# Optimization experiments

Hardware: AMD Instinct MI355X
Metric: run time of the kernel (lower is better)

The kernel has to match this reference:

```python
import jax, jax.numpy as jnp
import numpy as np

N = 65536          # particles
E = 524288         # relations (avg degree 8)
RIG = 4096         # rigid instance = particles [0, RIG); fluid = [RIG, N)
PSTEPS = 2
ATTR, STATE, RELD, NF = 3, 6, 1, 128
DT = 1.0 / 60.0
MEAN_P = np.zeros(3, np.float32); STD_P = np.ones(3, np.float32)
MEAN_V = np.zeros(3, np.float32); STD_V = np.ones(3, np.float32)


def _lin(x, w, b):
    return x @ w.T + b  # torch Linear convention: w is [out, in]


def setup_inputs() -> dict:
    key = jax.random.key(0)
    ks = iter(jax.random.split(key, 40))
    d = {}
    d["state"] = jax.random.normal(next(ks), (N, STATE), jnp.float32)
    d["attr"] = jax.random.normal(next(ks), (N, ATTR), jnp.float32)
    d["Ra"] = jax.random.normal(next(ks), (E, RELD), jnp.float32)
    d["rel_recv"] = jax.random.randint(next(ks), (E,), 0, N, jnp.int32)
    d["rel_send"] = jax.random.randint(next(ks), (E,), 0, N, jnp.int32)

    def w(shape):
        return jax.random.normal(next(ks), shape, jnp.float32) / np.sqrt(shape[1])

    d["pe_w0"] = w((NF, ATTR + 2 * STATE)); d["pe_b0"] = jnp.zeros(NF)
    d["pe_w1"] = w((NF, NF)); d["pe_b1"] = jnp.zeros(NF)
    d["re_w0"] = w((NF, 2 * ATTR + 4 * STATE + RELD)); d["re_b0"] = jnp.zeros(NF)
    d["re_w1"] = w((NF, NF)); d["re_b1"] = jnp.zeros(NF)
    d["re_w2"] = w((NF, NF)); d["re_b2"] = jnp.zeros(NF)
    d["rp_w"] = w((NF, 3 * NF)); d["rp_b"] = jnp.zeros(NF)
    d["pp_w"] = w((NF, 2 * NF)); d["pp_b"] = jnp.zeros(NF)
    d["rg_w0"] = w((NF, NF)); d["rg_b0"] = jnp.zeros(NF)
    d["rg_w1"] = w((NF, NF)); d["rg_b1"] = jnp.zeros(NF)
    d["rg_w2"] = w((7, NF)); d["rg_b2"] = jnp.zeros(7)
    d["fl_w0"] = w((NF, NF)); d["fl_b0"] = jnp.zeros(NF)
    d["fl_w1"] = w((NF, NF)); d["fl_b1"] = jnp.zeros(NF)
    d["fl_w2"] = w((3, NF)); d["fl_b2"] = jnp.zeros(3)
    return d


def reference(state, attr, Ra, rel_recv, rel_send,
              pe_w0, pe_b0, pe_w1, pe_b1,
              re_w0, re_b0, re_w1, re_b1, re_w2, re_b2,
              rp_w, rp_b, pp_w, pp_b,
              rg_w0, rg_b0, rg_w1, rg_b1, rg_w2, rg_b2,
              fl_w0, fl_b0, fl_w1, fl_b1, fl_w2, fl_b2):
    relu = jax.nn.relu
    mean_p = jnp.asarray(MEAN_P); std_p = jnp.asarray(STD_P)
    mean_v = jnp.asarray(MEAN_V); std_v = jnp.asarray(STD_V)

    # rigid-body offset (state minus instance centroid for the rigid instance)
    offset = jnp.zeros_like(state).at[:RIG].set(
        state[:RIG] - jnp.mean(state[:RIG], axis=0))
    attr2 = jnp.concatenate([attr, offset], axis=1)        # [N, ATTR+STATE]

    # f_O^enc: particle encoder on [attr2, state]
    pe_in = jnp.concatenate([attr2, state], axis=1)         # [N, 15]
    particle_encode = relu(_lin(relu(_lin(pe_in, pe_w0, pe_b0)), pe_w1, pe_b1))

    # f_R^enc: relation encoder on gathered receiver/sender features
    rel_in = jnp.concatenate([attr2[rel_recv], attr2[rel_send],
                              state[rel_recv], state[rel_send], Ra], axis=1)  # [E, 31]
    h = relu(_lin(rel_in, re_w0, re_b0))
    h = relu(_lin(h, re_w1, re_b1))
    relation_encode = relu(_lin(h, re_w2, re_b2))           # [E, NF]

    # propagation: gather effects -> f_R -> scatter-add -> f_O
    effect = jnp.zeros((N, NF), state.dtype)
    for _ in range(PSTEPS):
        r_eff = effect[rel_recv]                            # [E, NF]
        s_eff = effect[rel_send]                            # [E, NF]
        rel_eff = relu(_lin(jnp.concatenate(
            [relation_encode, r_eff, s_eff], axis=1), rp_w, rp_b))
        agg = jax.ops.segment_sum(rel_eff, rel_recv, num_segments=N)  # Rr @ rel_eff
        effect = relu(_lin(jnp.concatenate(
            [particle_encode, agg], axis=1), pp_w, pp_b))   # residual=False

    # rigid predictor: quaternion + translation of the rigid body
    pooled = jnp.mean(effect[:RIG], axis=0)                 # [NF]
    t = _lin(relu(_lin(relu(_lin(pooled, rg_w0, rg_b0)), rg_w1, rg_b1)), rg_w2, rg_b2)
    q = t[:4] / jnp.linalg.norm(t[:4])
    w, x, y, z = q[0], q[1], q[2], q[3]
    R = jnp.stack([
        jnp.stack([1.0 - 2 * (y * y + z * z), 2 * (x * y + z * w), 2 * (x * z - y * w)]),
        jnp.stack([2 * (x * y - z * w), 1.0 - 2 * (x * x + z * z), 2 * (y * z + x * w)]),
        jnp.stack([2 * (x * z + y * w), 2 * (y * z - x * w), 1.0 - 2 * (x * x + y * y)]),
    ])
    b = t[4:] * std_p
    p0 = state[:RIG, :3] * std_p + mean_p
    c = jnp.mean(p0, axis=0)
    p1 = (p0 - c) @ R + b + c
    v = (p1 - p0) / DT
    pred_rigid = (v - mean_v) / std_v                       # [RIG, 3]

    # fluid predictor: per-particle MLP
    f = relu(_lin(effect[RIG:], fl_w0, fl_b0))
    f = relu(_lin(f, fl_w1, fl_b1))
    pred_fluid = _lin(f, fl_w2, fl_b2)                      # [N-RIG, 3]

    return jnp.concatenate([pred_rigid, pred_fluid], axis=0)  # [N, 3]
```

## Files before the change

### kernel.cpp

```cpp
#include <hip/hip_runtime.h>
#include <hip/hip_bf16.h>
#include <cstdio>

#define N_P   65536
#define N_E   524288
#define RIG_  4096

typedef __attribute__((ext_vector_type(8))) short bf16x8;
typedef __attribute__((ext_vector_type(4))) float f32x4;
typedef unsigned short u16;
typedef unsigned int   u32;

__device__ __forceinline__ u16 f2b(float x) {
    __hip_bfloat16 h = __float2bfloat16(x);
    return *(u16*)&h;
}
__device__ __forceinline__ float b2f(u16 u) {
    union { unsigned u; float f; } c; c.u = ((unsigned)u) << 16; return c.f;
}
__device__ __forceinline__ unsigned pk2(float x, float y) {
    return (unsigned)f2b(x) | ((unsigned)f2b(y) << 16);
}
#define MFMA(a,b,c) __builtin_amdgcn_mfma_f32_16x16x32_bf16((a),(b),(c),0,0,0)

__device__ __forceinline__ void bar_l() {
    asm volatile("s_waitcnt lgkmcnt(0)\n\ts_barrier" ::: "memory");
}

__global__ __launch_bounds__(256) void k_hist(const int* __restrict__ recv,
                                              u32* __restrict__ cnt) {
    int i = blockIdx.x * 256 + threadIdx.x;
    if (i < N_E) atomicAdd(&cnt[recv[i]], 1u);
}
__global__ __launch_bounds__(256) void k_scan1(u32* __restrict__ data,
                                               u32* __restrict__ bsum) {
    __shared__ u32 s[256];
    int t = threadIdx.x, g = blockIdx.x * 256 + t;
    u32 v = data[g];
    s[t] = v; __syncthreads();
    for (int o = 1; o < 256; o <<= 1) {
        u32 x = (t >= o) ? s[t - o] : 0u;
        __syncthreads(); s[t] += x; __syncthreads();
    }
    data[g] = s[t] - v;
    if (t == 255) bsum[blockIdx.x] = s[255];
}
__global__ __launch_bounds__(256) void k_scan2(u32* __restrict__ bsum) {
    __shared__ u32 s[256];
    int t = threadIdx.x;
    u32 v = bsum[t];
    s[t] = v; __syncthreads();
    for (int o = 1; o < 256; o <<= 1) {
        u32 x = (t >= o) ? s[t - o] : 0u;
        __syncthreads(); s[t] += x; __syncthreads();
    }
    bsum[t] = s[t] - v;
}
__global__ __launch_bounds__(256) void k_scan3(u32* __restrict__ data,
                                               const u32* __restrict__ bsum) {
    int g = blockIdx.x * 256 + threadIdx.x;
    data[g] += bsum[blockIdx.x];
}
__global__ __launch_bounds__(256) void k_scatter(const int* __restrict__ recv,
                                                 const int* __restrict__ send,
                                                 u32* __restrict__ head,
                                                 int4* __restrict__ edges) {
    int i = blockIdx.x * 256 + threadIdx.x;
    if (i < N_E) {
        int n = recv[i];
        u32 pos = atomicAdd(&head[n], 1u);
        edges[pos] = make_int4(n, send[i], i, 0);
    }
}

struct CvtJob { const float* src; u16* dst; int n; int mode; int bstart; };
struct CvtArgs { CvtJob j[14]; };

__global__ __launch_bounds__(256) void k_cvt_all(CvtArgs a) {
    int b = blockIdx.x;
    int ji = 0;
    #pragma unroll
    for (int k = 1; k < 14; k++) if (b >= a.j[k].bstart) ji = k;
    CvtJob jb = a.j[ji];
    int i = (b - jb.bstart) * 256 + threadIdx.x;
    if (i >= jb.n) return;
    if (jb.mode == 0) {
        jb.dst[i] = f2b(jb.src[i]);
    } else if (jb.mode == 2) {
        int r = i >> 7;
        jb.dst[i] = (r < 3) ? f2b(jb.src[i]) : 0;
    } else if (jb.mode == 3) {
        int r = i >> 7, c = i & 127;
        jb.dst[i] = f2b(jb.src[r * 384 + c]);
    } else if (jb.mode == 4) {
        int r = i >> 7, c = i & 127;
        jb.dst[i] = f2b(jb.src[r * 256 + c]);
    } else if (jb.mode == 5) {
        int r = i >> 5, c = i & 31;
        float v = 0.f;
        if (c < 9)       v = jb.src[r * 31 + c];
        else if (c < 15) v = jb.src[r * 31 + 18 + (c - 9)];
        jb.dst[i] = f2b(v);
    } else if (jb.mode == 6) {
        int r = i >> 5, c = i & 31;
        float v = 0.f;
        if (c < 9)       v = jb.src[r * 31 + 9 + c];
        else if (c < 15) v = jb.src[r * 31 + 24 + (c - 9)];
        jb.dst[i] = f2b(v);
    } else {
        int r = i >> 5, c = i & 31;
        jb.dst[i] = (c < 15) ? f2b(jb.src[r * 15 + c]) : 0;
    }
}

__global__ __launch_bounds__(256) void k_centroid(const float* __restrict__ state,
                                                  float* __restrict__ cent) {
    int d = blockIdx.x;
    __shared__ float red[256];
    float s = 0.f;
    for (int r = threadIdx.x; r < RIG_; r += 256) s += state[r * 6 + d];
    red[threadIdx.x] = s; __syncthreads();
    for (int o = 128; o > 0; o >>= 1) {
        if (threadIdx.x < o) red[threadIdx.x] += red[threadIdx.x + o];
        __syncthreads();
    }
    if (threadIdx.x == 0) cent[d] = red[0] / (float)RIG_;
}

__global__ __launch_bounds__(512, 4) void k_particle_ext(
        const float* __restrict__ state, const float* __restrict__ attr,
        const float* __restrict__ cent,
        const u16* __restrict__ w0r, const u16* __restrict__ w0s,
        const u16* __restrict__ pew0, const float* __restrict__ pe_b0,
        const u16* __restrict__ pew1, const float* __restrict__ pe_b1,
        const u16* __restrict__ wp,
        u16* __restrict__ P, u16* __restrict__ Q, u16* __restrict__ T) {
    __shared__ float in_s[64][16];
    __shared__ u16 INF[64 * 32];
    __shared__ __align__(16) u16 BUFA[64 * 128];
    __shared__ __align__(16) u16 BUFB[64 * 128];
    int t = threadIdx.x;
    int w = t >> 6, lane = t & 63, mm = lane & 15, quad = lane >> 4;
    int colw = w * 16 + mm;
    bf16x8 W0Rf = *(const bf16x8*)(w0r  + (size_t)colw * 32 + quad * 8);
    bf16x8 W0Sf = *(const bf16x8*)(w0s  + (size_t)colw * 32 + quad * 8);
    bf16x8 PE0f = *(const bf16x8*)(pew0 + (size_t)colw * 32 + quad * 8);
    bf16x8 PE1f[4], WPf[4];
    #pragma unroll
    for (int kc = 0; kc < 4; kc++) {
        PE1f[kc] = *(const bf16x8*)(pew1 + (size_t)colw * 128 + kc * 32 + quad * 8);
        WPf[kc]  = *(const bf16x8*)(wp   + (size_t)colw * 128 + kc * 32 + quad * 8);
    }
    float b0c = pe_b0[colw], b1c = pe_b1[colw];
    const int NTL = N_P / 64;
    for (int tile = blockIdx.x; tile < NTL; tile += gridDim.x) {
        int base = tile * 64;
        bar_l();
        for (int it = t; it < 64 * 15; it += 512) {
            int r = it / 15, c = it % 15;
            int p = base + r;
            float v;
            if (c < 3)      v = attr[p * 3 + c];
            else if (c < 9) v = (p < RIG_) ? (state[p * 6 + (c - 3)] - cent[c - 3]) : 0.0f;
            else            v = state[p * 6 + (c - 9)];
            in_s[r][c] = v;
        }
        bar_l();
        if (t < 256) {
            int wv = t >> 6, kq4 = (t >> 4) & 3, m = t & 15;
            int e = wv * 16 + m;
            u16 tmp[8];
            #pragma unroll
            for (int j = 0; j < 8; j++) {
                int k = kq4 * 8 + j;
                tmp[j] = (k < 15) ? f2b(in_s[e][k]) : (u16)0;
            }
            *(uint4*)&INF[((wv * 4 + kq4) * 16 + m) * 8] = *(uint4*)tmp;
        }
        bar_l();
        bf16x8 af0[4];
        #pragma unroll
        for (int eg = 0; eg < 4; eg++)
            af0[eg] = *(const bf16x8*)&INF[((eg * 4 + quad) * 16 + mm) * 8];
        {
            f32x4 a[4] = {};
            #pragma unroll
            for (int eg = 0; eg < 4; eg++) a[eg] = MFMA(af0[eg], W0Rf, a[eg]);
            #pragma unroll
            for (int eg = 0; eg < 4; eg++)
                #pragma unroll
                for (int rg = 0; rg < 4; rg++)
                    P[(size_t)(base + eg * 16 + quad * 4 + rg) * 128 + colw] = f2b(a[eg][rg]);
        }
        {
            f32x4 a[4] = {};
            #pragma unroll
            for (int eg = 0; eg < 4; eg++) a[eg] = MFMA(af0[eg], W0Sf, a[eg]);
            #pragma unroll
            for (int eg = 0; eg < 4; eg++)
                #pragma unroll
                for (int rg = 0; rg < 4; rg++)
                    Q[(size_t)(base + eg * 16 + quad * 4 + rg) * 128 + colw] = f2b(a[eg][rg]);
        }
        {
            f32x4 a[4] = {};
            #pragma unroll
            for (int eg = 0; eg < 4; eg++) a[eg] = MFMA(af0[eg], PE0f, a[eg]);
            #pragma unroll
            for (int eg = 0; eg < 4; eg++)
                #pragma unroll
                for (int rg = 0; rg < 4; rg++)
                    BUFA[((eg * 16 + (colw >> 3)) * 16 + quad * 4 + rg) * 8 + (colw & 7)] =
                        f2b(fmaxf(a[eg][rg] + b0c, 0.f));
        }
        bar_l();
        {
            f32x4 a[4] = {};
            #pragma unroll
            for (int eg = 0; eg < 4; eg++)
                #pragma unroll
                for (int kc = 0; kc < 4; kc++) {
                    bf16x8 af = *(const bf16x8*)&BUFA[((eg * 16 + kc * 4 + quad) * 16 + mm) * 8];
                    a[eg] = MFMA(af, PE1f[kc], a[eg]);
                }
            #pragma unroll
            for (int eg = 0; eg < 4; eg++)
                #pragma unroll
                for (int rg = 0; rg < 4; rg++)
                    BUFB[((eg * 16 + (colw >> 3)) * 16 + quad * 4 + rg) * 8 + (colw & 7)] =
                        f2b(fmaxf(a[eg][rg] + b1c, 0.f));
        }
        bar_l();
        {
            f32x4 a[4] = {};
            #pragma unroll
            for (int eg = 0; eg < 4; eg++)
                #pragma unroll
                for (int kc = 0; kc < 4; kc++) {
                    bf16x8 af = *(const bf16x8*)&BUFB[((eg * 16 + kc * 4 + quad) * 16 + mm) * 8];
                    a[eg] = MFMA(af, WPf[kc], a[eg]);
                }
            #pragma unroll
            for (int eg = 0; eg < 4; eg++)
                #pragma unroll
                for (int rg = 0; rg < 4; rg++)
                    T[(size_t)(base + eg * 16 + quad * 4 + rg) * 128 + colw] = f2b(a[eg][rg]);
        }
    }
}

__global__ __launch_bounds__(512, 4) void k_rel(
        const u16* __restrict__ P, const u16* __restrict__ Q,
        const float* __restrict__ Ra, const int4* __restrict__ edges,
        const float* __restrict__ re_w0_raw, const float* __restrict__ b0,
        const u16* __restrict__ w1b, const float* __restrict__ b1,
        const u16* __restrict__ w2b, const float* __restrict__ b2,
        const u16* __restrict__ wreb, const float* __restrict__ rpb,
        u16* __restrict__ Z, float* __restrict__ agg) {
    __shared__ __align__(16) u16 BUFA[64 * 136];
    __shared__ __align__(16) u16 BUFB[64 * 136];
    __shared__ int rv_s[2][64];
    __shared__ float wRa_s[128], b0_s[128], rpb_s[128];
    int t = threadIdx.x;
    if (t < 128) {
        wRa_s[t] = re_w0_raw[t * 31 + 30];
        b0_s[t] = b0[t]; rpb_s[t] = rpb[t];
    }
    int w = t >> 6, lane = t & 63, mm = lane & 15, quad = lane >> 4;
    int colw = w * 16 + mm;
    bf16x8 W1f[4], W2f[4], WEf[4];
    #pragma unroll
    for (int kc = 0; kc < 4; kc++) {
        W1f[kc] = *(const bf16x8*)(w1b  + (size_t)colw * 128 + kc * 32 + quad * 8);
        W2f[kc] = *(const bf16x8*)(w2b  + (size_t)colw * 128 + kc * 32 + quad * 8);
        WEf[kc] = *(const bf16x8*)(wreb + (size_t)colw * 128 + kc * 32 + quad * 8);
    }
    float b1c = b1[colw], b2c = b2[colw];
    int es = t >> 3, cs2 = (t & 7) * 2;
    int egs = es >> 4, ms = es & 15;
    int sseg = t >> 7, cseg = t & 127;
    int zrow = t >> 3, zc0 = (t & 7) * 16;
    const long NT = N_E / 64;
    const long stride = gridDim.x;

    long tile = blockIdx.x;
    uint4 upC0, upC1, uqC0, uqC1; float raC; int rvC;
    {
        long nb = tile * 64;
        int4 e = edges[nb + es];
        rvC = edges[nb + (t & 63)].x;
        raC = Ra[e.z];
        upC0 = *(const uint4*)(P + (size_t)e.x * 128 + (size_t)cs2 * 8);
        upC1 = *(const uint4*)(P + (size_t)e.x * 128 + (size_t)(cs2 + 1) * 8);
        uqC0 = *(const uint4*)(Q + (size_t)e.y * 128 + (size_t)cs2 * 8);
        uqC1 = *(const uint4*)(Q + (size_t)e.y * 128 + (size_t)(cs2 + 1) * 8);
    }
    __syncthreads();
    int p = 0;
    for (; tile < NT; tile += stride) {
        long base = tile * 64;
        long ntile = tile + stride;
        bool hn = ntile < NT;
        int4 eN = make_int4(0, 0, 0, 0); int rvN = 0;
        if (hn) {
            long nb = ntile * 64;
            eN  = edges[nb + es];
            rvN = edges[nb + (t & 63)].x;
        }
        if (t < 64) rv_s[p][t] = rvC;
        {
            #pragma unroll
            for (int ci = 0; ci < 2; ci++) {
                int kq = cs2 + ci;
                uint4 up = ci ? upC1 : upC0;
                uint4 uq = ci ? uqC1 : uqC0;
                const u16* pp = (const u16*)&up; const u16* qq = (const u16*)&uq;
                u16 outv[8];
                #pragma unroll
                for (int j = 0; j < 8; j++) {
                    int c = kq * 8 + j;
                    float v = b2f(pp[j]) + b2f(qq[j]) + raC * wRa_s[c] + b0_s[c];
                    outv[j] = f2b(fmaxf(v, 0.f));
                }
                *(uint4*)&BUFA[((egs * 16 + kq) * 16 + ms) * 8] = *(uint4*)outv;
            }
        }
        bar_l();
        uint4 upN0{}, upN1{}, uqN0{}, uqN1{}; float raN = 0.f;
        if (hn) {
            raN  = Ra[eN.z];
            upN0 = *(const uint4*)(P + (size_t)eN.x * 128 + (size_t)cs2 * 8);
            upN1 = *(const uint4*)(P + (size_t)eN.x * 128 + (size_t)(cs2 + 1) * 8);
            uqN0 = *(const uint4*)(Q + (size_t)eN.y * 128 + (size_t)cs2 * 8);
            uqN1 = *(const uint4*)(Q + (size_t)eN.y * 128 + (size_t)(cs2 + 1) * 8);
        }
        {
            f32x4 acc[4] = {};
            #pragma unroll
            for (int eg = 0; eg < 4; eg++)
                #pragma unroll
                for (int kc = 0; kc < 4; kc++) {
                    bf16x8 af = *(const bf16x8*)&BUFA[((eg * 16 + kc * 4 + quad) * 16 + mm) * 8];
                    acc[eg] = MFMA(af, W1f[kc], acc[eg]);
                }
            #pragma unroll
            for (int eg = 0; eg < 4; eg++)
                #pragma unroll
                for (int rg = 0; rg < 4; rg++)
                    BUFB[((eg * 16 + (colw >> 3)) * 16 + quad * 4 + rg) * 8 + (colw & 7)] =
                        f2b(fmaxf(acc[eg][rg] + b1c, 0.f));
        }
        bar_l();
        {
            f32x4 acc[4] = {};
            #pragma unroll
            for (int eg = 0; eg < 4; eg++)
                #pragma unroll
                for (int kc = 0; kc < 4; kc++) {
                    bf16x8 af = *(const bf16x8*)&BUFB[((eg * 16 + kc * 4 + quad) * 16 + mm) * 8];
                    acc[eg] = MFMA(af, W2f[kc], acc[eg]);
                }
            #pragma unroll
            for (int eg = 0; eg < 4; eg++)
                #pragma unroll
                for (int rg = 0; rg < 4; rg++)
                    BUFA[((eg * 16 + (colw >> 3)) * 16 + quad * 4 + rg) * 8 + (colw & 7)] =
                        f2b(fmaxf(acc[eg][rg] + b2c, 0.f));
        }
        bar_l();
        {
            f32x4 zacc[4] = {};
            #pragma unroll
            for (int eg = 0; eg < 4; eg++)
                #pragma unroll
                for (int kc = 0; kc < 4; kc++) {
                    bf16x8 af = *(const bf16x8*)&BUFA[((eg * 16 + kc * 4 + quad) * 16 + mm) * 8];
                    zacc[eg] = MFMA(af, WEf[kc], zacc[eg]);
                }
            #pragma unroll
            for (int eg = 0; eg < 4; eg++)
                #pragma unroll
                for (int rg = 0; rg < 4; rg++)
                    BUFB[(eg * 16 + quad * 4 + rg) * 136 + colw] = f2b(zacc[eg][rg]);
        }
        bar_l();
        {
            uint4 z0 = *(const uint4*)&BUFB[zrow * 136 + zc0];
            uint4 z1 = *(const uint4*)&BUFB[zrow * 136 + zc0 + 8];
            *(uint4*)&Z[(base + zrow) * 128 + zc0]     = z0;
            *(uint4*)&Z[(base + zrow) * 128 + zc0 + 8] = z1;
        }
        {
            int r0 = sseg * 16;
            int cur = rv_s[p][r0];
            float a = fmaxf(b2f(BUFB[r0 * 136 + cseg]) + rpb_s[cseg], 0.f);
            bool first = true;
            for (int rr = r0 + 1; rr < r0 + 16; rr++) {
                int n = rv_s[p][rr];
                float v = fmaxf(b2f(BUFB[rr * 136 + cseg]) + rpb_s[cseg], 0.f);
                if (n == cur) a += v;
                else {
                    if (first) atomicAdd(&agg[(size_t)cur * 128 + cseg], a);
                    else       agg[(size_t)cur * 128 + cseg] = a;
                    first = false; cur = n; a = v;
                }
            }
            atomicAdd(&agg[(size_t)cur * 128 + cseg], a);
        }
        if (hn) { upC0 = upN0; upC1 = upN1; uqC0 = uqN0; uqC1 = uqN1; raC = raN; rvC = rvN; }
        p ^= 1;
    }
}

__global__ __launch_bounds__(512, 4) void k_node2(
        const float* __restrict__ agg, const u16* __restrict__ T,
        const u16* __restrict__ wab, const float* __restrict__ ppb,
        const u16* __restrict__ wrb, const u16* __restrict__ wsb,
        u16* __restrict__ U, u16* __restrict__ V) {
    __shared__ __align__(16) u16 BUFA[64 * 128];
    __shared__ __align__(16) u16 BUFB[64 * 128];
    int t = threadIdx.x;
    int w = t >> 6, lane = t & 63, mm = lane & 15, quad = lane >> 4;
    int colw = w * 16 + mm;
    bf16x8 WAf[4], WRf[4], WSf[4];
    #pragma unroll
    for (int kc = 0; kc < 4; kc++) {
        WAf[kc] = *(const bf16x8*)(wab + (size_t)colw * 128 + kc * 32 + quad * 8);
        WRf[kc] = *(const bf16x8*)(wrb + (size_t)colw * 128 + kc * 32 + quad * 8);
        WSf[kc] = *(const bf16x8*)(wsb + (size_t)colw * 128 + kc * 32 + quad * 8);
    }
    float ppbc = ppb[colw];
    int es = t >> 3, cs2 = (t & 7) * 2;
    int egs = es >> 4, ms = es & 15;
    const int NTL = N_P / 64;
    for (int tile = blockIdx.x; tile < NTL; tile += gridDim.x) {
        long base = (long)tile * 64;
        __syncthreads();
        #pragma unroll
        for (int ci = 0; ci < 2; ci++) {
            int kq = cs2 + ci;
            const float* src = agg + (base + es) * 128 + kq * 8;
            float4 f0 = *(const float4*)src, f1 = *(const float4*)(src + 4);
            uint4 v;
            v.x = pk2(f0.x, f0.y); v.y = pk2(f0.z, f0.w);
            v.z = pk2(f1.x, f1.y); v.w = pk2(f1.z, f1.w);
            *(uint4*)&BUFA[((egs * 16 + kq) * 16 + ms) * 8] = v;
        }
        bar_l();
        {
            f32x4 acc[4] = {};
            #pragma unroll
            for (int eg = 0; eg < 4; eg++)
                #pragma unroll
                for (int kc = 0; kc < 4; kc++) {
                    bf16x8 af = *(const bf16x8*)&BUFA[((eg * 16 + kc * 4 + quad) * 16 + mm) * 8];
                    acc[eg] = MFMA(af, WAf[kc], acc[eg]);
                }
            #pragma unroll
            for (int eg = 0; eg < 4; eg++)
                #pragma unroll
                for (int rg = 0; rg < 4; rg++) {
                    long row = base + eg * 16 + quad * 4 + rg;
                    float v = acc[eg][rg] + b2f(T[row * 128 + colw]) + ppbc;
                    BUFB[((eg * 16 + (colw >> 3)) * 16 + quad * 4 + rg) * 8 + (colw & 7)] =
                        f2b(fmaxf(v, 0.f));
                }
        }
        bar_l();
        {
            f32x4 au[4] = {}, av[4] = {};
            #pragma unroll
            for (int eg = 0; eg < 4; eg++)
                #pragma unroll
                for (int kc = 0; kc < 4; kc++) {
                    bf16x8 af = *(const bf16x8*)&BUFB[((eg * 16 + kc * 4 + quad) * 16 + mm) * 8];
                    au[eg] = MFMA(af, WRf[kc], au[eg]);
                    av[eg] = MFMA(af, WSf[kc], av[eg]);
                }
            #pragma unroll
            for (int eg = 0; eg < 4; eg++)
                #pragma unroll
                for (int rg = 0; rg < 4; rg++) {
                    long row = base + eg * 16 + quad * 4 + rg;
                    U[row * 128 + colw] = f2b(au[eg][rg]);
                    V[row * 128 + colw] = f2b(av[eg][rg]);
                }
        }
    }
}

__global__ __launch_bounds__(512, 4) void k_node2fl(
        const float* __restrict__ agg, const u16* __restrict__ T,
        const u16* __restrict__ wab, const float* __restrict__ ppb,
        float* __restrict__ pooledsum,
        const u16* __restrict__ w0b, const float* __restrict__ b0,
        const u16* __restrict__ w1b, const float* __restrict__ b1,
        const u16* __restrict__ w2b, const float* __restrict__ b2,
        float* __restrict__ out) {
    __shared__ __align__(16) u16 BUFA[64 * 128];
    __shared__ __align__(16) u16 BUFB[64 * 128];
    int t = threadIdx.x;
    int w = t >> 6, lane = t & 63, mm = lane & 15, quad = lane >> 4;
    int colw = w * 16 + mm;
    bf16x8 WAf[4], W0f[4], W1f[4];
    #pragma unroll
    for (int kc = 0; kc < 4; kc++) {
        WAf[kc] = *(const bf16x8*)(wab + (size_t)colw * 128 + kc * 32 + quad * 8);
        W0f[kc] = *(const bf16x8*)(w0b + (size_t)colw * 128 + kc * 32 + quad * 8);
        W1f[kc] = *(const bf16x8*)(w1b + (size_t)colw * 128 + kc * 32 + quad * 8);
    }
    float ppbc = ppb[colw], b0c = b0[colw], b1c = b1[colw];
    int es = t >> 3, cs2 = (t & 7) * 2;
    int egs = es >> 4, ms = es & 15;
    const int NTL = N_P / 64;
    for (int tile = blockIdx.x; tile < NTL; tile += gridDim.x) {
        long base = (long)tile * 64;
        bool fluid = base >= RIG_;
        bar_l();
        #pragma unroll
        for (int ci = 0; ci < 2; ci++) {
            int kq = cs2 + ci;
            const float* src = agg + (base + es) * 128 + kq * 8;
            float4 f0 = *(const float4*)src, f1 = *(const float4*)(src + 4);
            uint4 v;
            v.x = pk2(f0.x, f0.y); v.y = pk2(f0.z, f0.w);
            v.z = pk2(f1.x, f1.y); v.w = pk2(f1.z, f1.w);
            *(uint4*)&BUFA[((egs * 16 + kq) * 16 + ms) * 8] = v;
        }
        bar_l();
        f32x4 acc[4] = {};
        #pragma unroll
        for (int eg = 0; eg < 4; eg++)
            #pragma unroll
            for (int kc = 0; kc < 4; kc++) {
                bf16x8 af = *(const bf16x8*)&BUFA[((eg * 16 + kc * 4 + quad) * 16 + mm) * 8];
                acc[eg] = MFMA(af, WAf[kc], acc[eg]);
            }
        if (!fluid) {
            float s = 0.f;
            #pragma unroll
            for (int eg = 0; eg < 4; eg++)
                #pragma unroll
                for (int rg = 0; rg < 4; rg++) {
                    long row = base + eg * 16 + quad * 4 + rg;
                    float v = acc[eg][rg] + b2f(T[row * 128 + colw]) + ppbc;
                    s += b2f(f2b(fmaxf(v, 0.f)));
                }
            s += __shfl_xor(s, 16);
            s += __shfl_xor(s, 32);
            if (quad == 0) atomicAdd(&pooledsum[colw], s);
            continue;
        }
        #pragma unroll
        for (int eg = 0; eg < 4; eg++)
            #pragma unroll
            for (int rg = 0; rg < 4; rg++) {
                long row = base + eg * 16 + quad * 4 + rg;
                float v = acc[eg][rg] + b2f(T[row * 128 + colw]) + ppbc;
                BUFB[((eg * 16 + (colw >> 3)) * 16 + quad * 4 + rg) * 8 + (colw & 7)] =
                    f2b(fmaxf(v, 0.f));
            }
        bar_l();
        {
            f32x4 a[4] = {};
            #pragma unroll
            for (int eg = 0; eg < 4; eg++)
                #pragma unroll
                for (int kc = 0; kc < 4; kc++) {
                    bf16x8 af = *(const bf16x8*)&BUFB[((eg * 16 + kc * 4 + quad) * 16 + mm) * 8];
                    a[eg] = MFMA(af, W0f[kc], a[eg]);
                }
            #pragma unroll
            for (int eg = 0; eg < 4; eg++)
                #pragma unroll
                for (int rg = 0; rg < 4; rg++)
                    BUFA[((eg * 16 + (colw >> 3)) * 16 + quad * 4 + rg) * 8 + (colw & 7)] =
                        f2b(fmaxf(a[eg][rg] + b0c, 0.f));
        }
        bar_l();
        {
            f32x4 a[4] = {};
            #pragma unroll
            for (int eg = 0; eg < 4; eg++)
                #pragma unroll
                for (int kc = 0; kc < 4; kc++) {
                    bf16x8 af = *(const bf16x8*)&BUFA[((eg * 16 + kc * 4 + quad) * 16 + mm) * 8];
                    a[eg] = MFMA(af, W1f[kc], a[eg]);
                }
            #pragma unroll
            for (int eg = 0; eg < 4; eg++)
                #pragma unroll
                for (int rg = 0; rg < 4; rg++)
                    BUFB[((eg * 16 + (colw >> 3)) * 16 + quad * 4 + rg) * 8 + (colw & 7)] =
                        f2b(fmaxf(a[eg][rg] + b1c, 0.f));
        }
        bar_l();
        if (w < 4) {
            f32x4 a1 = {};
            #pragma unroll
            for (int kc = 0; kc < 4; kc++) {
                bf16x8 af = *(const bf16x8*)&BUFB[((w * 16 + kc * 4 + quad) * 16 + mm) * 8];
                bf16x8 bf = *(const bf16x8*)(w2b + (size_t)mm * 128 + kc * 32 + quad * 8);
                a1 = MFMA(af, bf, a1);
            }
            if (mm < 3) {
                float bv = b2[mm];
                #pragma unroll
                for (int rg = 0; rg < 4; rg++) {
                    long row = base + w * 16 + quad * 4 + rg;
                    out[row * 3 + mm] = a1[rg] + bv;
                }
            }
        }
    }
}

__global__ __launch_bounds__(256) void k_edge2(
        const u16* __restrict__ Z, const u16* __restrict__ U, const u16* __restrict__ V,
        const int4* __restrict__ edges,
        const float* __restrict__ rpb, float* __restrict__ agg) {
    __shared__ __align__(16) u16 S16[64 * 136];
    __shared__ int rv_s[64];
    __shared__ float rpb_s[128];
    int t = threadIdx.x;
    long base = (long)blockIdx.x * 64;
    if (t < 64) rv_s[t] = edges[base + t].x;
    if (t < 128) rpb_s[t] = rpb[t];
    int r = t >> 2, q = t & 3;
    int4 er = edges[base + r];
    long zb = (base + r) * 128;
    size_t ub = (size_t)er.x * 128, vb = (size_t)er.y * 128;
    bar_l();
    #pragma unroll
    for (int i = 0; i < 4; i++) {
        int c0 = q * 32 + i * 8;
        uint4 uz = *(const uint4*)(Z + zb + c0);
        uint4 uu = *(const uint4*)(U + ub + c0);
        uint4 uv = *(const uint4*)(V + vb + c0);
        const u16* zz = (const u16*)&uz; const u16* pu = (const u16*)&uu; const u16* pv = (const u16*)&uv;
        u16 o[8];
        #pragma unroll
        for (int j = 0; j < 8; j++)
            o[j] = f2b(fmaxf(b2f(zz[j]) + b2f(pu[j]) + b2f(pv[j]) + rpb_s[c0 + j], 0.f));
        *(uint4*)&S16[r * 136 + c0] = *(uint4*)o;
    }
    bar_l();
    {
        int s = t >> 7, col = t & 127;
        int r0 = s * 32;
        int cur = rv_s[r0];
        float a = b2f(S16[r0 * 136 + col]);
        bool first = true;
        for (int rr = r0 + 1; rr < r0 + 32; rr++) {
            int n = rv_s[rr];
            float v = b2f(S16[rr * 136 + col]);
            if (n == cur) a += v;
            else {
                if (first) atomicAdd(&agg[(size_t)cur * 128 + col], a);
                else       agg[(size_t)cur * 128 + col] = a;
                first = false; cur = n; a = v;
            }
        }
        atomicAdd(&agg[(size_t)cur * 128 + col], a);
    }
}

__global__ __launch_bounds__(128) void k_rigid_head(
        const float* __restrict__ pooledsum,
        const float* __restrict__ w0, const float* __restrict__ b0,
        const float* __restrict__ w1, const float* __restrict__ b1,
        const float* __restrict__ w2, const float* __restrict__ b2,
        float* __restrict__ rig) {
    __shared__ float pl[128], ha[128], hb[128], tv[7];
    int t = threadIdx.x;
    pl[t] = pooledsum[t] * (1.0f / (float)RIG_);
    __syncthreads();
    float a = b0[t];
    for (int k = 0; k < 128; k++) a += w0[t * 128 + k] * pl[k];
    ha[t] = fmaxf(a, 0.f);
    __syncthreads();
    a = b1[t];
    for (int k = 0; k < 128; k++) a += w1[t * 128 + k] * ha[k];
    hb[t] = fmaxf(a, 0.f);
    __syncthreads();
    if (t < 7) {
        float s = b2[t];
        for (int k = 0; k < 128; k++) s += w2[t * 128 + k] * hb[k];
        tv[t] = s;
    }
    __syncthreads();
    if (t == 0) {
        float w = tv[0], x = tv[1], y = tv[2], z = tv[3];
        float n = sqrtf(w * w + x * x + y * y + z * z);
        w /= n; x /= n; y /= n; z /= n;
        rig[0] = 1.f - 2.f * (y * y + z * z); rig[1] = 2.f * (x * y + z * w); rig[2] = 2.f * (x * z - y * w);
        rig[3] = 2.f * (x * y - z * w); rig[4] = 1.f - 2.f * (x * x + z * z); rig[5] = 2.f * (y * z + x * w);
        rig[6] = 2.f * (x * z + y * w); rig[7] = 2.f * (y * z - x * w); rig[8] = 1.f - 2.f * (x * x + y * y);
        rig[9] = tv[4]; rig[10] = tv[5]; rig[11] = tv[6];
    }
}

__global__ __launch_bounds__(256) void k_rigid_out(
        const float* __restrict__ state, const float* __restrict__ cent,
        const float* __restrict__ rig, float* __restrict__ out) {
    int i = blockIdx.x * 256 + threadIdx.x;
    if (i >= RIG_) return;
    float p0[3], d[3];
    #pragma unroll
    for (int k = 0; k < 3; k++) { p0[k] = state[i * 6 + k]; d[k] = p0[k] - cent[k]; }
    #pragma unroll
    for (int j = 0; j < 3; j++) {
        float p1 = rig[0 * 3 + j] * d[0] + rig[1 * 3 + j] * d[1] + rig[2 * 3 + j] * d[2]
                 + rig[9 + j] + cent[j];
        out[i * 3 + j] = (p1 - p0[j]) * 60.0f;
    }
}

extern "C" void kernel_launch(void* const* d_in, const int* in_sizes, int n_in,
                              void* d_out, int out_size, void* d_ws, size_t ws_size,
                              hipStream_t stream) {
    const float* state = (const float*)d_in[0];
    const float* attr  = (const float*)d_in[1];
    const float* Ra    = (const float*)d_in[2];
    const int*   recv  = (const int*)d_in[3];
    const int*   send  = (const int*)d_in[4];
    const float* pe_w0 = (const float*)d_in[5];  const float* pe_b0 = (const float*)d_in[6];
    const float* pe_w1 = (const float*)d_in[7];  const float* pe_b1 = (const float*)d_in[8];
    const float* re_w0 = (const float*)d_in[9];  const float* re_b0 = (const float*)d_in[10];
    const float* re_w1 = (const float*)d_in[11]; const float* re_b1 = (const float*)d_in[12];
    const float* re_w2 = (const float*)d_in[13]; const float* re_b2 = (const float*)d_in[14];
    const float* rp_w  = (const float*)d_in[15]; const float* rp_b  = (const float*)d_in[16];
    const float* pp_w  = (const float*)d_in[17]; const float* pp_b  = (const float*)d_in[18];
    const float* rg_w0 = (const float*)d_in[19]; const float* rg_b0 = (const float*)d_in[20];
    const float* rg_w1 = (const float*)d_in[21]; const float* rg_b1 = (const float*)d_in[22];
    const float* rg_w2 = (const float*)d_in[23]; const float* rg_b2 = (const float*)d_in[24];
    const float* fl_w0 = (const float*)d_in[25]; const float* fl_b0 = (const float*)d_in[26];
    const float* fl_w1 = (const float*)d_in[27]; const float* fl_b1 = (const float*)d_in[28];
    const float* fl_w2 = (const float*)d_in[29]; const float* fl_b2 = (const float*)d_in[30];
    float* out = (float*)d_out;

    char* p = (char*)d_ws;
    auto alloc = [&](size_t bytes) { char* r = p; p += (bytes + 255) / 256 * 256; return r; };
    float* cent    = (float*)alloc(8 * 4);
    float* pooled  = (float*)alloc(128 * 4);
    float* rig     = (float*)alloc(16 * 4);
    u32*   rowhead = (u32*)alloc((size_t)N_P * 4);
    u32*   bsum    = (u32*)alloc(256 * 4);
    int4*  edges   = (int4*)alloc((size_t)N_E * 16);
    float* agg     = (float*)alloc((size_t)N_P * 128 * 4);
    u16*   Z       = (u16*)alloc((size_t)N_E * 128 * 2);
    u16*   T       = (u16*)alloc((size_t)N_P * 128 * 2);
    u16*   P       = (u16*)alloc((size_t)N_P * 128 * 2);
    u16*   Q       = (u16*)alloc((size_t)N_P * 128 * 2);
    u16*   wreb    = (u16*)alloc(128 * 128 * 2);
    u16*   wrb     = (u16*)alloc(128 * 128 * 2);
    u16*   wsb     = (u16*)alloc(128 * 128 * 2);
    u16*   wpb     = (u16*)alloc(128 * 128 * 2);
    u16*   wab     = (u16*)alloc(128 * 128 * 2);
    u16*   rw1b    = (u16*)alloc(128 * 128 * 2);
    u16*   rw2b    = (u16*)alloc(128 * 128 * 2);
    u16*   pew1b   = (u16*)alloc(128 * 128 * 2);
    u16*   flw0b   = (u16*)alloc(128 * 128 * 2);
    u16*   flw1b   = (u16*)alloc(128 * 128 * 2);
    u16*   flw2b   = (u16*)alloc(16 * 128 * 2);
    u16*   w0rb    = (u16*)alloc(128 * 32 * 2);
    u16*   w0sb    = (u16*)alloc(128 * 32 * 2);
    u16*   pew0b   = (u16*)alloc(128 * 32 * 2);
    size_t need = (size_t)(p - (char*)d_ws);
    if (ws_size < need) {
        fprintf(stderr, "kernel_launch: ws_size %zu < needed %zu\n", ws_size, need);
        return;
    }
    u16* U = P; u16* V = Q;

    hipMemsetAsync(rowhead, 0, (size_t)N_P * 4, stream);
    k_hist<<<N_E / 256, 256, 0, stream>>>(recv, rowhead);
    k_scan1<<<N_P / 256, 256, 0, stream>>>(rowhead, bsum);
    k_scan2<<<1, 256, 0, stream>>>(bsum);
    k_scan3<<<N_P / 256, 256, 0, stream>>>(rowhead, bsum);
    k_scatter<<<N_E / 256, 256, 0, stream>>>(recv, send, rowhead, edges);

    CvtArgs ca;
    int bs = 0;
    auto addjob = [&](int idx, const float* s, u16* d, int n, int mode) {
        ca.j[idx] = {s, d, n, mode, bs};
        bs += (n + 255) / 256;
    };
    addjob(0,  rp_w,        wreb,  128 * 128, 3);
    addjob(1,  rp_w + 128,  wrb,   128 * 128, 3);
    addjob(2,  rp_w + 256,  wsb,   128 * 128, 3);
    addjob(3,  pp_w,        wpb,   128 * 128, 4);
    addjob(4,  pp_w + 128,  wab,   128 * 128, 4);
    addjob(5,  re_w1,       rw1b,  128 * 128, 0);
    addjob(6,  re_w2,       rw2b,  128 * 128, 0);
    addjob(7,  pe_w1,       pew1b, 128 * 128, 0);
    addjob(8,  fl_w0,       flw0b, 128 * 128, 0);
    addjob(9,  fl_w1,       flw1b, 128 * 128, 0);
    addjob(10, fl_w2,       flw2b, 16 * 128,  2);
    addjob(11, re_w0,       w0rb,  128 * 32,  5);
    addjob(12, re_w0,       w0sb,  128 * 32,  6);
    addjob(13, pe_w0,       pew0b, 128 * 32,  7);
    k_cvt_all<<<bs, 256, 0, stream>>>(ca);

    k_centroid<<<6, 256, 0, stream>>>(state, cent);
    k_particle_ext<<<512, 512, 0, stream>>>(state, attr, cent,
                                            w0rb, w0sb, pew0b, pe_b0,
                                            pew1b, pe_b1, wpb, P, Q, T);

    hipMemsetAsync(agg, 0, (size_t)N_P * 128 * 4, stream);
    k_rel<<<512, 512, 0, stream>>>(P, Q, Ra, edges,
                                   re_w0, re_b0, rw1b, re_b1, rw2b, re_b2,
                                   wreb, rp_b, Z, agg);
    k_node2<<<512, 512, 0, stream>>>(agg, T, wab, pp_b, wrb, wsb, U, V);

    hipMemsetAsync(agg, 0, (size_t)N_P * 128 * 4, stream);
    hipMemsetAsync(pooled, 0, 128 * 4, stream);
    k_edge2<<<N_E / 64, 256, 0, stream>>>(Z, U, V, edges, rp_b, agg);
    k_node2fl<<<512, 512, 0, stream>>>(agg, T, wab, pp_b, pooled,
                                       flw0b, fl_b0, flw1b, fl_b1,
                                       flw2b, fl_b2, out);

    k_rigid_head<<<1, 128, 0, stream>>>(pooled, rg_w0, rg_b0, rg_w1, rg_b1, rg_w2, rg_b2, rig);
    k_rigid_out<<<(RIG_ + 255) / 256, 256, 0, stream>>>(state, cent, rig, out);
}
```

Baseline: 467.6 us.

## Make edge2 kernel persistent with register prefetch and double-buffered LDS

k_edge2 becomes a grid-stride persistent kernel with 512 blocks of 512 threads. Each thread loads the next 64-edge tile's Z/U/V gathers and receiver ids into registers while the current tile is combined and segment-reduced from a double-buffered shared tile. This is meant to hide gather latency and cut block launch overhead, and it needs only one barrier per tile. In exchange, reduction segments shrink from 32 to 16 rows, which raises the number of boundary atomics to agg, and register pressure grows.

```diff
diff --git a/kernel.cpp b/kernel.cpp
--- a/kernel.cpp
+++ b/kernel.cpp
@@ -615,53 +615,85 @@
     }
 }
 
-__global__ __launch_bounds__(256) void k_edge2(
+__global__ __launch_bounds__(512, 4) void k_edge2(
         const u16* __restrict__ Z, const u16* __restrict__ U, const u16* __restrict__ V,
         const int4* __restrict__ edges,
         const float* __restrict__ rpb, float* __restrict__ agg) {
-    __shared__ __align__(16) u16 S16[64 * 136];
-    __shared__ int rv_s[64];
+    __shared__ __align__(16) u16 S16[2][64 * 136];
+    __shared__ int rv_s[2][64];
     __shared__ float rpb_s[128];
     int t = threadIdx.x;
-    long base = (long)blockIdx.x * 64;
-    if (t < 64) rv_s[t] = edges[base + t].x;
     if (t < 128) rpb_s[t] = rpb[t];
-    int r = t >> 2, q = t & 3;
-    int4 er = edges[base + r];
-    long zb = (base + r) * 128;
-    size_t ub = (size_t)er.x * 128, vb = (size_t)er.y * 128;
-    bar_l();
-    #pragma unroll
-    for (int i = 0; i < 4; i++) {
-        int c0 = q * 32 + i * 8;
-        uint4 uz = *(const uint4*)(Z + zb + c0);
-        uint4 uu = *(const uint4*)(U + ub + c0);
-        uint4 uv = *(const uint4*)(V + vb + c0);
-        const u16* zz = (const u16*)&uz; const u16* pu = (const u16*)&uu; const u16* pv = (const u16*)&uv;
-        u16 o[8];
-        #pragma unroll
-        for (int j = 0; j < 8; j++)
-            o[j] = f2b(fmaxf(b2f(zz[j]) + b2f(pu[j]) + b2f(pv[j]) + rpb_s[c0 + j], 0.f));
-        *(uint4*)&S16[r * 136 + c0] = *(uint4*)o;
-    }
-    bar_l();
+    int ec = t >> 3, cc = (t & 7) * 16;
+    int sseg = t >> 7, cseg = t & 127;
+    const long NT = N_E / 64;
+    const long stride = gridDim.x;
+
+    long tile = blockIdx.x;
+    uint4 zC0, zC1, uC0, uC1, vC0, vC1; int rvC;
     {
-        int s = t >> 7, col = t & 127;
-        int r0 = s * 32;
-        int cur = rv_s[r0];
-        float a = b2f(S16[r0 * 136 + col]);
-        bool first = true;
-        for (int rr = r0 + 1; rr < r0 + 32; rr++) {
-            int n = rv_s[rr];
-            float v = b2f(S16[rr * 136 + col]);
-            if (n == cur) a += v;
-            else {
-                if (first) atomicAdd(&agg[(size_t)cur * 128 + col], a);
-                else       agg[(size_t)cur * 128 + col] = a;
-                first = false; cur = n; a = v;
+        long nb = tile * 64;
+        int4 e = edges[nb + ec];
+        rvC = edges[nb + (t & 63)].x;
+        const u16* zp = Z + (nb + ec) * 128 + cc;
+        zC0 = *(const uint4*)zp; zC1 = *(const uint4*)(zp + 8);
+        const u16* up = U + (size_t)e.x * 128 + cc;
+        uC0 = *(const uint4*)up; uC1 = *(const uint4*)(up + 8);
+        const u16* vp = V + (size_t)e.y * 128 + cc;
+        vC0 = *(const uint4*)vp; vC1 = *(const uint4*)(vp + 8);
+    }
+    __syncthreads();
+    int p = 0;
+    for (; tile < NT; tile += stride) {
+        long ntile = tile + stride;
+        bool hn = ntile < NT;
+        if (t < 64) rv_s[p][t] = rvC;
+        {
+            const u16* zz = (const u16*)&zC0; const u16* uu = (const u16*)&uC0;
+            const u16* vv = (const u16*)&vC0;
+            u16 o[8];
+            #pragma unroll
+            for (int j = 0; j < 8; j++)
+                o[j] = f2b(fmaxf(b2f(zz[j]) + b2f(uu[j]) + b2f(vv[j]) + rpb_s[cc + j], 0.f));
+            *(uint4*)&S16[p][ec * 136 + cc] = *(uint4*)o;
+            zz = (const u16*)&zC1; uu = (const u16*)&uC1; vv = (const u16*)&vC1;
+            #pragma unroll
+            for (int j = 0; j < 8; j++)
+                o[j] = f2b(fmaxf(b2f(zz[j]) + b2f(uu[j]) + b2f(vv[j]) + rpb_s[cc + 8 + j], 0.f));
+            *(uint4*)&S16[p][ec * 136 + cc + 8] = *(uint4*)o;
+        }
+        uint4 zN0{}, zN1{}, uN0{}, uN1{}, vN0{}, vN1{}; int rvN = 0;
+        if (hn) {
+            long nb = ntile * 64;
+            int4 e = edges[nb + ec];
+            rvN = edges[nb + (t & 63)].x;
+            const u16* zp = Z + (nb + ec) * 128 + cc;
+            zN0 = *(const uint4*)zp; zN1 = *(const uint4*)(zp + 8);
+            const u16* up = U + (size_t)e.x * 128 + cc;
+            uN0 = *(const uint4*)up; uN1 = *(const uint4*)(up + 8);
+            const u16* vp = V + (size_t)e.y * 128 + cc;
+            vN0 = *(const uint4*)vp; vN1 = *(const uint4*)(vp + 8);
+        }
+        bar_l();
+        {
+            int r0 = sseg * 16;
+            int cur = rv_s[p][r0];
+            float a = b2f(S16[p][r0 * 136 + cseg]);
+            bool first = true;
+            for (int rr = r0 + 1; rr < r0 + 16; rr++) {
+                int n = rv_s[p][rr];
+                float v = b2f(S16[p][rr * 136 + cseg]);
+                if (n == cur) a += v;
+                else {
+                    if (first) atomicAdd(&agg[(size_t)cur * 128 + cseg], a);
+                    else       agg[(size_t)cur * 128 + cseg] = a;
+                    first = false; cur = n; a = v;
+                }
             }
-        }
-        atomicAdd(&agg[(size_t)cur * 128 + col], a);
+            atomicAdd(&agg[(size_t)cur * 128 + cseg], a);
+        }
+        if (hn) { zC0 = zN0; zC1 = zN1; uC0 = uN0; uC1 = uN1; vC0 = vN0; vC1 = vN1; rvC = rvN; }
+        p ^= 1;
     }
 }
 
@@ -815,7 +847,7 @@
 
     hipMemsetAsync(agg, 0, (size_t)N_P * 128 * 4, stream);
     hipMemsetAsync(pooled, 0, 128 * 4, stream);
-    k_edge2<<<N_E / 64, 256, 0, stream>>>(Z, U, V, edges, rp_b, agg);
+    k_edge2<<<512, 512, 0, stream>>>(Z, U, V, edges, rp_b, agg);
     k_node2fl<<<512, 512, 0, stream>>>(agg, T, wab, pp_b, pooled,
                                        flw0b, fl_b0, flw1b, fl_b1,
                                        flw2b, fl_b2, out);
```

Result: no change. 462.2 us (-1.2%).
